# Performance work log

Measured on AMD Instinct MI355X. Metric: run time of the kernel, lower is better.

The kernel has to match this reference:

```python
import jax, jax.numpy as jnp
import numpy as np

D_IN = 1024
D_OUT = 1024
NUM_HEADS = 16
HEAD_DIM = D_OUT // NUM_HEADS
CONTEXT_LEN = 2048


def setup_inputs() -> dict:
    key = jax.random.key(0)
    ks = jax.random.split(key, 7)
    scale = 0.02
    x = jax.random.normal(ks[0], (2, 2048, D_IN), dtype=jnp.float32)
    Wq = jax.random.normal(ks[1], (D_IN, D_OUT), dtype=jnp.float32) * scale
    bq = jnp.zeros((D_OUT,), dtype=jnp.float32)
    Wk = jax.random.normal(ks[2], (D_IN, D_OUT), dtype=jnp.float32) * scale
    bk = jnp.zeros((D_OUT,), dtype=jnp.float32)
    Wv = jax.random.normal(ks[3], (D_IN, D_OUT), dtype=jnp.float32) * scale
    bv = jnp.zeros((D_OUT,), dtype=jnp.float32)
    return {"x": x, "Wq": Wq, "bq": bq, "Wk": Wk, "bk": bk, "Wv": Wv, "bv": bv}


def reference(x, Wq, bq, Wk, bk, Wv, bv):
    B, S, _ = x.shape
    # QKV projections with bias
    q = x @ Wq + bq  # [B,S,D_OUT]
    k = x @ Wk + bk
    v = x @ Wv + bv
    # split heads -> [B,H,S,Dh]
    def heads(t):
        return t.reshape(B, S, NUM_HEADS, HEAD_DIM).transpose(0, 2, 1, 3)
    q, k, v = heads(q), heads(k), heads(v)
    # raw scores, then additive causal mask (-1e9 on strictly upper triangle),
    # then scale by 1/sqrt(head_dim) AFTER adding mask (matches original code)
    scores = jnp.einsum("bhqd,bhkd->bhqk", q, k)
    causal = jnp.tril(jnp.ones((S, S), dtype=bool))
    add_mask = jnp.where(causal, 0.0, -1e9).astype(scores.dtype)
    scores = scores + add_mask
    weights = jax.nn.softmax(scores / jnp.sqrt(jnp.asarray(HEAD_DIM, scores.dtype)), axis=-1)
    ctx = jnp.einsum("bhqk,bhkd->bhqd", weights, v)  # [B,H,S,Dh]
    return ctx.transpose(0, 2, 1, 3).reshape(B, S, D_OUT)
```

## Files before the change

### kernel.cpp

```cpp
#include <hip/hip_runtime.h>
#include <hip/hip_bf16.h>
#include <stdint.h>

#define D_IN 1024
#define NH 16
#define DH 64
#define SEQ 2048
#define BATCH 2

typedef unsigned short u16;
typedef __attribute__((ext_vector_type(8))) short short8;
typedef __attribute__((ext_vector_type(4))) float f32x4;

#define CSCALE 0.1803368801f

__device__ __forceinline__ u16 f2bf(float f) {
    union { float f; uint32_t u; } v; v.f = f;
    uint32_t r = v.u + 0x7FFF + ((v.u >> 16) & 1);
    return (u16)(r >> 16);
}

__device__ __forceinline__ float bf2f(u16 u) {
    union { uint32_t u; float f; } v; v.u = (uint32_t)u << 16;
    return v.f;
}

__device__ __forceinline__ uint32_t pktrunc(float a, float b) {
    union { float f; uint32_t u; } x, y;
    x.f = a; y.f = b;
    return __builtin_amdgcn_perm(y.u, x.u, 0x07060302u);
}

__device__ __forceinline__ void async16(const u16* g, u16* l) {
    __builtin_amdgcn_global_load_lds(
        (const __attribute__((address_space(1))) void*)g,
        (__attribute__((address_space(3))) void*)l, 16, 0, 0);
}

__global__ __launch_bounds__(256) void prep_kernel(
    const float* __restrict__ x, const float* __restrict__ Wq,
    const float* __restrict__ Wk, const float* __restrict__ Wv,
    u16* __restrict__ xb, u16* __restrict__ WT)
{
    __shared__ float tile[64][65];
    if (blockIdx.x < 4096) {
        int i = (blockIdx.x * 256 + threadIdx.x) * 4;
        float4 v = *(const float4*)(x + i);
        union { u16 u[4]; uint2 d; } o;
        o.u[0] = f2bf(v.x); o.u[1] = f2bf(v.y); o.u[2] = f2bf(v.z); o.u[3] = f2bf(v.w);
        *(uint2*)(xb + i) = o.d;
        return;
    }
    int idx = blockIdx.x - 4096;
    int mat = idx >> 8, rem = idx & 255;
    int k0 = (rem & 15) * 64, n0 = (rem >> 4) * 64;
    const float* W = (mat == 0) ? Wq : (mat == 1 ? Wk : Wv);
    int c = threadIdx.x & 63, rb = threadIdx.x >> 6;
    #pragma unroll
    for (int p = 0; p < 16; ++p) {
        int r = p * 4 + rb;
        tile[r][c] = W[(size_t)(k0 + r) * 1024 + n0 + c];
    }
    __syncthreads();
    #pragma unroll
    for (int p = 0; p < 16; ++p) {
        int r = p * 4 + rb;
        WT[((size_t)mat * 1024 + n0 + r) * 1024 + k0 + c] = f2bf(tile[c][r]);
    }
}

__global__ __launch_bounds__(256) void qkv_gemm_kernel(
    const u16* __restrict__ xb, const u16* __restrict__ WT,
    const float* __restrict__ bq, const float* __restrict__ bk,
    const float* __restrict__ bv,
    u16* __restrict__ Qb, u16* __restrict__ Kb, u16* __restrict__ Vh)
{
    __shared__ u16 As[128 * 32];
    __shared__ u16 Bs[128 * 32];
    const int tid  = threadIdx.x;
    const int wave = tid >> 6, lane = tid & 63;
    const int quad = lane >> 4, l15 = lane & 15;
    const int m0 = blockIdx.y * 128;
    const int n0 = blockIdx.x * 128;

    f32x4 acc[4][4];
    #pragma unroll
    for (int i = 0; i < 4; ++i)
        #pragma unroll
        for (int j = 0; j < 4; ++j)
            acc[i][j] = (f32x4){0.f, 0.f, 0.f, 0.f};

    const int wm = wave & 1, wn = wave >> 1;
    const int srow = wave * 32 + (lane >> 2);
    const int scol = (lane & 3) * 8;

    for (int k0 = 0; k0 < 1024; k0 += 32) {
        #pragma unroll
        for (int t = 0; t < 2; ++t) {
            int row = srow + t * 16;
            async16(xb + (size_t)(m0 + row) * 1024 + k0 + scol, As + row * 32 + scol);
            async16(WT + (size_t)(n0 + row) * 1024 + k0 + scol, Bs + row * 32 + scol);
        }
        __syncthreads();
        short8 af[4], bfr[4];
        #pragma unroll
        for (int f = 0; f < 4; ++f) {
            af[f]  = *(const short8*)(As + (wm * 64 + f * 16 + l15) * 32 + quad * 8);
            bfr[f] = *(const short8*)(Bs + (wn * 64 + f * 16 + l15) * 32 + quad * 8);
        }
        #pragma unroll
        for (int i = 0; i < 4; ++i)
            #pragma unroll
            for (int j = 0; j < 4; ++j)
                acc[i][j] = __builtin_amdgcn_mfma_f32_16x16x32_bf16(af[i], bfr[j], acc[i][j], 0, 0, 0);
        __syncthreads();
    }

    const int mat = n0 >> 10;
    const float* bias = (mat == 0) ? bq : (mat == 1 ? bk : bv);
    u16* dst = (mat == 0) ? Qb : (mat == 1 ? Kb : Vh);
    const float sc = (mat == 0) ? CSCALE : 1.0f;
    const int ncb = (n0 & 1023) + wn * 64;
    const int hh = ncb >> 6;
    #pragma unroll
    for (int i = 0; i < 4; ++i) {
        int gm = m0 + wm * 64 + i * 16 + quad * 4;
        int bb = gm >> 11, ss = gm & 2047;
        #pragma unroll
        for (int j = 0; j < 4; ++j) {
            int dh = j * 16 + l15;
            float bval = bias[ncb + dh];
            size_t base = (((size_t)bb * NH + hh) * SEQ + ss) * DH + dh;
            #pragma unroll
            for (int r = 0; r < 4; ++r)
                dst[base + (size_t)r * DH] = f2bf((acc[i][j][r] + bval) * sc);
        }
    }
}

__global__ __launch_bounds__(256) void transpose_v_kernel(
    const u16* __restrict__ Vh, u16* __restrict__ Vt)
{
    __shared__ uint32_t tile[64][65];
    int s0 = blockIdx.x * 64;
    size_t bh = blockIdx.y;
    int c = threadIdx.x & 63, rb = threadIdx.x >> 6;
    const u16* src = Vh + (bh * SEQ + s0) * DH;
    #pragma unroll
    for (int p = 0; p < 16; ++p) {
        int r = p * 4 + rb;
        tile[r][c] = src[(size_t)r * DH + c];
    }
    __syncthreads();
    u16* dst = Vt + bh * DH * SEQ + s0;
    #pragma unroll
    for (int p = 0; p < 16; ++p) {
        int d = p * 4 + rb;
        dst[(size_t)d * SEQ + c] = (u16)tile[c][d];
    }
}

__device__ __forceinline__ void stage64(const u16* g0, size_t gstride, u16* lds,
                                        int wave, int lane)
{
    #pragma unroll
    for (int rnd = 0; rnd < 2; ++rnd) {
        int row = rnd * 32 + wave * 8 + (lane >> 3);
        int c = (lane & 7) ^ (row & 7);
        async16(g0 + (size_t)row * gstride + c * 8, lds + row * 64 + (lane & 7) * 8);
    }
}

__global__ __launch_bounds__(256) void flash_mfma_kernel(
    const u16* __restrict__ Qb, const u16* __restrict__ Kb,
    const u16* __restrict__ Vt, float* __restrict__ out,
    u16* __restrict__ Opart, float* __restrict__ Lpart)
{
    static const int JQT[24] = {7,15,15,14,14, 6,13,13,12,12, 5,11,11,10,10,
                                4, 9, 9, 8, 8, 3, 2, 1, 0};
    static const int JHF[24] = {-1,0,1,0,1, -1,0,1,0,1, -1,0,1,0,1,
                                -1,0,1,0,1, -1,-1,-1,-1};

    __shared__ u16 Ks[2][64 * 64];
    __shared__ u16 Vs[2][64 * 64];
    __shared__ u16 Ps[128 * 76];

    const int tid  = threadIdx.x;
    const int wave = tid >> 6, lane = tid & 63;
    const int quad = lane >> 4, l15 = lane & 15;
    const int bhx = blockIdx.x;
    const int b = bhx >> 4, h = bhx & 15;
    const int job = blockIdx.y;
    const int qt = JQT[job], hf = JHF[job];
    const int t0 = (hf == 1) ? qt + 1 : 0;
    const int t1 = (hf == 0) ? qt + 1 : 2 * qt + 2;
    const int q0 = qt * 128;
    const int wq0 = wave * 32;
    const size_t bh = (size_t)bhx;
    const u16* Qp = Qb + bh * SEQ * DH;
    const u16* Kp = Kb + bh * SEQ * DH;
    const u16* Vp = Vt + bh * DH * SEQ;

    short8 qf[2][2];
    #pragma unroll
    for (int qa = 0; qa < 2; ++qa) {
        const u16* qrp = Qp + (size_t)(q0 + wq0 + qa * 16 + l15) * DH;
        qf[qa][0] = *(const short8*)(qrp + quad * 8);
        qf[qa][1] = *(const short8*)(qrp + 32 + quad * 8);
    }

    const short8 ones = (short8){0x3F80, 0x3F80, 0x3F80, 0x3F80,
                                 0x3F80, 0x3F80, 0x3F80, 0x3F80};

    f32x4 O[2][4], L[2];
    #pragma unroll
    for (int pa = 0; pa < 2; ++pa) {
        #pragma unroll
        for (int f = 0; f < 4; ++f) O[pa][f] = (f32x4){0.f, 0.f, 0.f, 0.f};
        L[pa] = (f32x4){0.f, 0.f, 0.f, 0.f};
    }

    const int wqmax = q0 + wq0 + 31;
    const int xq = l15 & 7;

    stage64(Kp + (size_t)t0 * 64 * DH, DH, Ks[t0 & 1], wave, lane);
    stage64(Vp + t0 * 64, SEQ, Vs[t0 & 1], wave, lane);
    __syncthreads();

    for (int t = t0; t < t1; ++t) {
        const int cur = t & 1;
        if (t + 1 < t1) {
            int k1 = (t + 1) * 64;
            stage64(Kp + (size_t)k1 * DH, DH, Ks[cur ^ 1], wave, lane);
            stage64(Vp + k1, SEQ, Vs[cur ^ 1], wave, lane);
        }
        const int k0 = t * 64;
        if (k0 <= wqmax) {
            f32x4 sf[4][2];
            #pragma unroll
            for (int fj = 0; fj < 4; ++fj) {
                const u16* krow = &Ks[cur][(fj * 16 + l15) * 64];
                short8 k0f = *(const short8*)(krow + (quad ^ xq) * 8);
                short8 k1f = *(const short8*)(krow + ((4 + quad) ^ xq) * 8);
                #pragma unroll
                for (int qa = 0; qa < 2; ++qa) {
                    f32x4 s = (f32x4){0.f, 0.f, 0.f, 0.f};
                    s = __builtin_amdgcn_mfma_f32_16x16x32_bf16(k0f, qf[qa][0], s, 0, 0, 0);
                    s = __builtin_amdgcn_mfma_f32_16x16x32_bf16(k1f, qf[qa][1], s, 0, 0, 0);
                    sf[fj][qa] = s;
                }
            }
            const bool diag = (k0 + 63 > q0 + wq0);
            #pragma unroll
            for (int fj = 0; fj < 4; ++fj)
                #pragma unroll
                for (int qa = 0; qa < 2; ++qa)
                    #pragma unroll
                    for (int r = 0; r < 4; ++r) {
                        float p = __builtin_amdgcn_exp2f(sf[fj][qa][r]);
                        if (diag) {
                            int key = k0 + fj * 16 + quad * 4 + r;
                            int qg  = q0 + wq0 + qa * 16 + l15;
                            p = (key <= qg) ? p : 0.f;
                        }
                        sf[fj][qa][r] = p;
                    }
            #pragma unroll
            for (int qa = 0; qa < 2; ++qa) {
                u16* prow = &Ps[(wq0 + qa * 16 + l15) * 76];
                #pragma unroll
                for (int fj = 0; fj < 4; ++fj) {
                    uint2 d;
                    d.x = pktrunc(sf[fj][qa][0], sf[fj][qa][1]);
                    d.y = pktrunc(sf[fj][qa][2], sf[fj][qa][3]);
                    *(uint2*)(prow + fj * 16 + quad * 4) = d;
                }
            }
            short8 pfr[2][2];
            #pragma unroll
            for (int pa = 0; pa < 2; ++pa) {
                const u16* prow = &Ps[(wq0 + pa * 16 + l15) * 76];
                pfr[pa][0] = *(const short8*)(prow + quad * 8);
                pfr[pa][1] = *(const short8*)(prow + 32 + quad * 8);
            }
            #pragma unroll
            for (int pa = 0; pa < 2; ++pa) {
                L[pa] = __builtin_amdgcn_mfma_f32_16x16x32_bf16(pfr[pa][0], ones, L[pa], 0, 0, 0);
                L[pa] = __builtin_amdgcn_mfma_f32_16x16x32_bf16(pfr[pa][1], ones, L[pa], 0, 0, 0);
            }
            #pragma unroll
            for (int fo = 0; fo < 4; ++fo) {
                const u16* vrow = &Vs[cur][(fo * 16 + l15) * 64];
                short8 vb0 = *(const short8*)(vrow + (quad ^ xq) * 8);
                short8 vb1 = *(const short8*)(vrow + ((4 + quad) ^ xq) * 8);
                #pragma unroll
                for (int pa = 0; pa < 2; ++pa) {
                    O[pa][fo] = __builtin_amdgcn_mfma_f32_16x16x32_bf16(pfr[pa][0], vb0, O[pa][fo], 0, 0, 0);
                    O[pa][fo] = __builtin_amdgcn_mfma_f32_16x16x32_bf16(pfr[pa][1], vb1, O[pa][fo], 0, 0, 0);
                }
            }
        }
        __syncthreads();
    }

    if (hf < 0) {
        #pragma unroll
        for (int pa = 0; pa < 2; ++pa)
            #pragma unroll
            for (int fo = 0; fo < 4; ++fo)
                #pragma unroll
                for (int r = 0; r < 4; ++r) {
                    int s = q0 + wq0 + pa * 16 + quad * 4 + r;
                    out[((size_t)b * SEQ + s) * 1024 + h * DH + fo * 16 + l15] =
                        O[pa][fo][r] / L[pa][r];
                }
    } else {
        const int pi = (qt - 8) * 2 + hf;
        u16* op = Opart + (((size_t)pi * 32 + bhx) * 128) * 64;
        float* lp = Lpart + ((size_t)pi * 32 + bhx) * 128;
        #pragma unroll
        for (int pa = 0; pa < 2; ++pa) {
            #pragma unroll
            for (int fo = 0; fo < 4; ++fo)
                #pragma unroll
                for (int r = 0; r < 4; ++r) {
                    int ql = wq0 + pa * 16 + quad * 4 + r;
                    op[(size_t)ql * 64 + fo * 16 + l15] = f2bf(O[pa][fo][r]);
                }
            if (l15 == 0) {
                #pragma unroll
                for (int r = 0; r < 4; ++r)
                    lp[wq0 + pa * 16 + quad * 4 + r] = L[pa][r];
            }
        }
    }
}

__global__ __launch_bounds__(256) void combine_kernel(
    const u16* __restrict__ Opart, const float* __restrict__ Lpart,
    float* __restrict__ out)
{
    int blk = blockIdx.x;
    int qt = 8 + (blk >> 5);
    int bh = blk & 31;
    int b = bh >> 4, h = bh & 15;
    int pi0 = (qt - 8) * 2, pi1 = pi0 + 1;
    int tid = threadIdx.x;
    int q = tid >> 1, seg = (tid & 1) * 32;
    const u16* o0 = Opart + (((size_t)pi0 * 32 + bh) * 128 + q) * 64 + seg;
    const u16* o1 = Opart + (((size_t)pi1 * 32 + bh) * 128 + q) * 64 + seg;
    float inv = 1.0f / (Lpart[((size_t)pi0 * 32 + bh) * 128 + q] +
                        Lpart[((size_t)pi1 * 32 + bh) * 128 + q]);
    float* op = out + ((size_t)b * SEQ + qt * 128 + q) * 1024 + h * DH + seg;
    #pragma unroll
    for (int d = 0; d < 32; d += 4) {
        union { uint2 d2; u16 u[4]; } a, c;
        a.d2 = *(const uint2*)(o0 + d);
        c.d2 = *(const uint2*)(o1 + d);
        float4 v;
        v.x = (bf2f(a.u[0]) + bf2f(c.u[0])) * inv;
        v.y = (bf2f(a.u[1]) + bf2f(c.u[1])) * inv;
        v.z = (bf2f(a.u[2]) + bf2f(c.u[2])) * inv;
        v.w = (bf2f(a.u[3]) + bf2f(c.u[3])) * inv;
        *(float4*)(op + d) = v;
    }
}

extern "C" void kernel_launch(void* const* d_in, const int* in_sizes, int n_in,
                              void* d_out, int out_size, void* d_ws, size_t ws_size,
                              hipStream_t stream) {
    const float* x  = (const float*)d_in[0];
    const float* Wq = (const float*)d_in[1];
    const float* bq = (const float*)d_in[2];
    const float* Wk = (const float*)d_in[3];
    const float* bk = (const float*)d_in[4];
    const float* Wv = (const float*)d_in[5];
    const float* bv = (const float*)d_in[6];
    float* out = (float*)d_out;

    const size_t NX = (size_t)BATCH * SEQ * D_IN;
    const size_t NW = (size_t)3 * D_IN * 1024;
    const size_t NP = (size_t)BATCH * NH * SEQ * DH;
    u16* xb = (u16*)d_ws;
    u16* WT = xb + NX;
    u16* Qb = WT + NW;
    u16* Kb = Qb + NP;
    u16* Vh = Kb + NP;
    u16* Vt = Vh + NP;
    u16* Opart = xb;
    float* Lpart = (float*)(xb + NX);

    prep_kernel<<<4096 + 768, 256, 0, stream>>>(x, Wq, Wk, Wv, xb, WT);
    qkv_gemm_kernel<<<dim3(24, 32), 256, 0, stream>>>(xb, WT, bq, bk, bv, Qb, Kb, Vh);
    transpose_v_kernel<<<dim3(SEQ / 64, BATCH * NH), 256, 0, stream>>>(Vh, Vt);
    flash_mfma_kernel<<<dim3(32, 24), 256, 0, stream>>>(Qb, Kb, Vt, out, Opart, Lpart);
    combine_kernel<<<256, 256, 0, stream>>>(Opart, Lpart, out);
}
```

Before: 170.8 us.

## Fuse V transpose into QKV GEMM epilogue and keep P in registers

The QKV GEMM epilogue now writes V directly in transposed layout through a per-wave LDS staging tile, which removes the separate transpose kernel and its round trip of V through global memory. In the flash kernel, the K rows are permuted and the LDS swizzle is changed so that the QK^T accumulator layout matches the A-operand layout of the PV MFMA. That lets P be packed straight from registers instead of going through the Ps shared buffer. In exchange, the GEMM epilogue gets more complex, and the new swizzle and row permutation must be exactly right for correctness.

```diff
diff --git a/kernel.cpp b/kernel.cpp
--- a/kernel.cpp
+++ b/kernel.cpp
@@ -73,10 +73,11 @@
     const u16* __restrict__ xb, const u16* __restrict__ WT,
     const float* __restrict__ bq, const float* __restrict__ bk,
     const float* __restrict__ bv,
-    u16* __restrict__ Qb, u16* __restrict__ Kb, u16* __restrict__ Vh)
-{
-    __shared__ u16 As[128 * 32];
-    __shared__ u16 Bs[128 * 32];
+    u16* __restrict__ Qb, u16* __restrict__ Kb, u16* __restrict__ Vt)
+{
+    __shared__ u16 smem[4 * 64 * 72];
+    u16* As = smem;
+    u16* Bs = smem + 128 * 32;
     const int tid  = threadIdx.x;
     const int wave = tid >> 6, lane = tid & 63;
     const int quad = lane >> 4, l15 = lane & 15;
@@ -117,46 +118,48 @@
     }
 
     const int mat = n0 >> 10;
-    const float* bias = (mat == 0) ? bq : (mat == 1 ? bk : bv);
-    u16* dst = (mat == 0) ? Qb : (mat == 1 ? Kb : Vh);
-    const float sc = (mat == 0) ? CSCALE : 1.0f;
     const int ncb = (n0 & 1023) + wn * 64;
     const int hh = ncb >> 6;
-    #pragma unroll
-    for (int i = 0; i < 4; ++i) {
-        int gm = m0 + wm * 64 + i * 16 + quad * 4;
-        int bb = gm >> 11, ss = gm & 2047;
-        #pragma unroll
-        for (int j = 0; j < 4; ++j) {
-            int dh = j * 16 + l15;
-            float bval = bias[ncb + dh];
-            size_t base = (((size_t)bb * NH + hh) * SEQ + ss) * DH + dh;
-            #pragma unroll
-            for (int r = 0; r < 4; ++r)
-                dst[base + (size_t)r * DH] = f2bf((acc[i][j][r] + bval) * sc);
-        }
-    }
-}
-
-__global__ __launch_bounds__(256) void transpose_v_kernel(
-    const u16* __restrict__ Vh, u16* __restrict__ Vt)
-{
-    __shared__ uint32_t tile[64][65];
-    int s0 = blockIdx.x * 64;
-    size_t bh = blockIdx.y;
-    int c = threadIdx.x & 63, rb = threadIdx.x >> 6;
-    const u16* src = Vh + (bh * SEQ + s0) * DH;
-    #pragma unroll
-    for (int p = 0; p < 16; ++p) {
-        int r = p * 4 + rb;
-        tile[r][c] = src[(size_t)r * DH + c];
-    }
-    __syncthreads();
-    u16* dst = Vt + bh * DH * SEQ + s0;
-    #pragma unroll
-    for (int p = 0; p < 16; ++p) {
-        int d = p * 4 + rb;
-        dst[(size_t)d * SEQ + c] = (u16)tile[c][d];
+    const int bb = m0 >> 11, sb = m0 & 2047;
+
+    if (mat < 2) {
+        const float* bias = (mat == 0) ? bq : bk;
+        u16* dst = (mat == 0) ? Qb : Kb;
+        const float sc = (mat == 0) ? CSCALE : 1.0f;
+        #pragma unroll
+        for (int i = 0; i < 4; ++i) {
+            int ss = sb + wm * 64 + i * 16 + quad * 4;
+            #pragma unroll
+            for (int j = 0; j < 4; ++j) {
+                int dh = j * 16 + l15;
+                float bval = bias[ncb + dh];
+                size_t base = (((size_t)bb * NH + hh) * SEQ + ss) * DH + dh;
+                #pragma unroll
+                for (int r = 0; r < 4; ++r)
+                    dst[base + (size_t)r * DH] = f2bf((acc[i][j][r] + bval) * sc);
+            }
+        }
+    } else {
+        u16* vt = smem + wave * (64 * 72);
+        #pragma unroll
+        for (int i = 0; i < 4; ++i)
+            #pragma unroll
+            for (int j = 0; j < 4; ++j) {
+                float bval = bv[ncb + j * 16 + l15];
+                union { u16 u[4]; uint2 d; } o;
+                #pragma unroll
+                for (int r = 0; r < 4; ++r)
+                    o.u[r] = f2bf(acc[i][j][r] + bval);
+                *(uint2*)(vt + (j * 16 + l15) * 72 + i * 16 + quad * 4) = o.d;
+            }
+        const int s0w = sb + wm * 64;
+        u16* vdst = Vt + ((size_t)(bb * NH + hh) * DH) * SEQ;
+        #pragma unroll
+        for (int it = 0; it < 8; ++it) {
+            int dh = it * 8 + (lane >> 3);
+            short8 v = *(const short8*)(vt + dh * 72 + (lane & 7) * 8);
+            *(short8*)(vdst + (size_t)dh * SEQ + s0w + (lane & 7) * 8) = v;
+        }
     }
 }
 
@@ -166,7 +169,8 @@
     #pragma unroll
     for (int rnd = 0; rnd < 2; ++rnd) {
         int row = rnd * 32 + wave * 8 + (lane >> 3);
-        int c = (lane & 7) ^ (row & 7);
+        int sig = ((row >> 3) & 1) * 4 + (row & 3);
+        int c = (lane & 7) ^ sig;
         async16(g0 + (size_t)row * gstride + c * 8, lds + row * 64 + (lane & 7) * 8);
     }
 }
@@ -183,7 +187,6 @@
 
     __shared__ u16 Ks[2][64 * 64];
     __shared__ u16 Vs[2][64 * 64];
-    __shared__ u16 Ps[128 * 76];
 
     const int tid  = threadIdx.x;
     const int wave = tid >> 6, lane = tid & 63;
@@ -221,7 +224,9 @@
     }
 
     const int wqmax = q0 + wq0 + 31;
-    const int xq = l15 & 7;
+    const int krbase = (l15 >> 2) * 8 + (l15 & 3);
+    const int ksig   = ((l15 >> 2) & 1) * 4 + (l15 & 3);
+    const int vsig   = ((l15 >> 3) & 1) * 4 + (l15 & 3);
 
     stage64(Kp + (size_t)t0 * 64 * DH, DH, Ks[t0 & 1], wave, lane);
     stage64(Vp + t0 * 64, SEQ, Vs[t0 & 1], wave, lane);
@@ -239,9 +244,10 @@
             f32x4 sf[4][2];
             #pragma unroll
             for (int fj = 0; fj < 4; ++fj) {
-                const u16* krow = &Ks[cur][(fj * 16 + l15) * 64];
-                short8 k0f = *(const short8*)(krow + (quad ^ xq) * 8);
-                short8 k1f = *(const short8*)(krow + ((4 + quad) ^ xq) * 8);
+                int krow = (fj >> 1) * 32 + krbase + (fj & 1) * 4;
+                const u16* kp = &Ks[cur][krow * 64];
+                short8 k0f = *(const short8*)(kp + (quad ^ ksig) * 8);
+                short8 k1f = *(const short8*)(kp + ((4 + quad) ^ ksig) * 8);
                 #pragma unroll
                 for (int qa = 0; qa < 2; ++qa) {
                     f32x4 s = (f32x4){0.f, 0.f, 0.f, 0.f};
@@ -251,52 +257,44 @@
                 }
             }
             const bool diag = (k0 + 63 > q0 + wq0);
-            #pragma unroll
-            for (int fj = 0; fj < 4; ++fj)
-                #pragma unroll
-                for (int qa = 0; qa < 2; ++qa)
+            short8 pA[2][2];
+            #pragma unroll
+            for (int qa = 0; qa < 2; ++qa) {
+                #pragma unroll
+                for (int fj = 0; fj < 4; ++fj)
                     #pragma unroll
                     for (int r = 0; r < 4; ++r) {
                         float p = __builtin_amdgcn_exp2f(sf[fj][qa][r]);
                         if (diag) {
-                            int key = k0 + fj * 16 + quad * 4 + r;
+                            int key = k0 + (fj >> 1) * 32 + quad * 8 + (fj & 1) * 4 + r;
                             int qg  = q0 + wq0 + qa * 16 + l15;
                             p = (key <= qg) ? p : 0.f;
                         }
                         sf[fj][qa][r] = p;
                     }
-            #pragma unroll
-            for (int qa = 0; qa < 2; ++qa) {
-                u16* prow = &Ps[(wq0 + qa * 16 + l15) * 76];
-                #pragma unroll
-                for (int fj = 0; fj < 4; ++fj) {
-                    uint2 d;
-                    d.x = pktrunc(sf[fj][qa][0], sf[fj][qa][1]);
-                    d.y = pktrunc(sf[fj][qa][2], sf[fj][qa][3]);
-                    *(uint2*)(prow + fj * 16 + quad * 4) = d;
-                }
-            }
-            short8 pfr[2][2];
-            #pragma unroll
-            for (int pa = 0; pa < 2; ++pa) {
-                const u16* prow = &Ps[(wq0 + pa * 16 + l15) * 76];
-                pfr[pa][0] = *(const short8*)(prow + quad * 8);
-                pfr[pa][1] = *(const short8*)(prow + 32 + quad * 8);
-            }
-            #pragma unroll
-            for (int pa = 0; pa < 2; ++pa) {
-                L[pa] = __builtin_amdgcn_mfma_f32_16x16x32_bf16(pfr[pa][0], ones, L[pa], 0, 0, 0);
-                L[pa] = __builtin_amdgcn_mfma_f32_16x16x32_bf16(pfr[pa][1], ones, L[pa], 0, 0, 0);
+                union { uint32_t d[4]; short8 v; } a0, a1;
+                a0.d[0] = pktrunc(sf[0][qa][0], sf[0][qa][1]);
+                a0.d[1] = pktrunc(sf[0][qa][2], sf[0][qa][3]);
+                a0.d[2] = pktrunc(sf[1][qa][0], sf[1][qa][1]);
+                a0.d[3] = pktrunc(sf[1][qa][2], sf[1][qa][3]);
+                a1.d[0] = pktrunc(sf[2][qa][0], sf[2][qa][1]);
+                a1.d[1] = pktrunc(sf[2][qa][2], sf[2][qa][3]);
+                a1.d[2] = pktrunc(sf[3][qa][0], sf[3][qa][1]);
+                a1.d[3] = pktrunc(sf[3][qa][2], sf[3][qa][3]);
+                pA[qa][0] = a0.v;
+                pA[qa][1] = a1.v;
+                L[qa] = __builtin_amdgcn_mfma_f32_16x16x32_bf16(pA[qa][0], ones, L[qa], 0, 0, 0);
+                L[qa] = __builtin_amdgcn_mfma_f32_16x16x32_bf16(pA[qa][1], ones, L[qa], 0, 0, 0);
             }
             #pragma unroll
             for (int fo = 0; fo < 4; ++fo) {
                 const u16* vrow = &Vs[cur][(fo * 16 + l15) * 64];
-                short8 vb0 = *(const short8*)(vrow + (quad ^ xq) * 8);
-                short8 vb1 = *(const short8*)(vrow + ((4 + quad) ^ xq) * 8);
+                short8 vb0 = *(const short8*)(vrow + (quad ^ vsig) * 8);
+                short8 vb1 = *(const short8*)(vrow + ((4 + quad) ^ vsig) * 8);
                 #pragma unroll
                 for (int pa = 0; pa < 2; ++pa) {
-                    O[pa][fo] = __builtin_amdgcn_mfma_f32_16x16x32_bf16(pfr[pa][0], vb0, O[pa][fo], 0, 0, 0);
-                    O[pa][fo] = __builtin_amdgcn_mfma_f32_16x16x32_bf16(pfr[pa][1], vb1, O[pa][fo], 0, 0, 0);
+                    O[pa][fo] = __builtin_amdgcn_mfma_f32_16x16x32_bf16(pA[pa][0], vb0, O[pa][fo], 0, 0, 0);
+                    O[pa][fo] = __builtin_amdgcn_mfma_f32_16x16x32_bf16(pA[pa][1], vb1, O[pa][fo], 0, 0, 0);
                 }
             }
         }
@@ -385,14 +383,12 @@
     u16* WT = xb + NX;
     u16* Qb = WT + NW;
     u16* Kb = Qb + NP;
-    u16* Vh = Kb + NP;
-    u16* Vt = Vh + NP;
+    u16* Vt = Kb + NP;
     u16* Opart = xb;
     float* Lpart = (float*)(xb + NX);
 
     prep_kernel<<<4096 + 768, 256, 0, stream>>>(x, Wq, Wk, Wv, xb, WT);
-    qkv_gemm_kernel<<<dim3(24, 32), 256, 0, stream>>>(xb, WT, bq, bk, bv, Qb, Kb, Vh);
-    transpose_v_kernel<<<dim3(SEQ / 64, BATCH * NH), 256, 0, stream>>>(Vh, Vt);
+    qkv_gemm_kernel<<<dim3(24, 32), 256, 0, stream>>>(xb, WT, bq, bk, bv, Qb, Kb, Vt);
     flash_mfma_kernel<<<dim3(32, 24), 256, 0, stream>>>(Qb, Kb, Vt, out, Opart, Lpart);
     combine_kernel<<<256, 256, 0, stream>>>(Opart, Lpart, out);
 }
```

After: 168.2 us. Within noise of the previous version (-1.6%).
